# Kernel optimization log

Hardware: AMD Instinct MI355X
Metric: run time of the kernel (lower is better)

Reference implementation:

```python
import jax, jax.numpy as jnp
import numpy as np

HEADS = 16
DIM_HEAD = 64
DIM = 1024
INNER = HEADS * DIM_HEAD  # 1024


def setup_inputs() -> dict:
    key = jax.random.key(0)
    ks = jax.random.split(key, 8)
    B, N, M = 4, 2048, 2048
    x = jax.random.normal(ks[0], (B, N, DIM), dtype=jnp.float32)
    context = jax.random.normal(ks[1], (B, M, DIM), dtype=jnp.float32)
    x_mask = (jax.random.uniform(ks[2], (B, N)) > 0.1).astype(jnp.float32)
    context_mask = (jax.random.uniform(ks[3], (B, M)) > 0.1).astype(jnp.float32)
    s = 0.02
    Wq = jax.random.normal(ks[4], (DIM, INNER), dtype=jnp.float32) * s
    Wkv = jax.random.normal(ks[5], (DIM, 2 * INNER), dtype=jnp.float32) * s
    Wo = jax.random.normal(ks[6], (INNER, DIM), dtype=jnp.float32) * s
    bo = jnp.zeros((DIM,), dtype=jnp.float32)
    return {"x": x, "context": context, "x_mask": x_mask,
            "context_mask": context_mask, "Wq": Wq, "Wkv": Wkv, "Wo": Wo, "bo": bo}


def _split_heads(t):
    b, n, _ = t.shape
    return t.reshape(b, n, HEADS, DIM_HEAD).transpose(0, 2, 1, 3)  # b h n d


def reference(x, context, x_mask, context_mask, Wq, Wkv, Wo, bo):
    scale = DIM_HEAD ** -0.5
    q = _split_heads(x @ Wq)                       # b h n d
    kv = context @ Wkv
    k = _split_heads(kv[..., :INNER])              # b h m d
    v = _split_heads(kv[..., INNER:])              # b h m d
    dots = jnp.einsum('bhnd,bhmd->bhnm', q, k) * scale
    # attn_bias = 1 - x_mask ⊗ context_mask; masked where isclose(attn_bias, 1)
    prod = x_mask[:, None, :, None] * context_mask[:, None, None, :]  # b 1 n m
    masked = jnp.isclose(1.0 - prod, 1.0)          # b 1 n m, broadcast over heads
    dots = jnp.where(masked, -jnp.inf, dots)       # b h n m
    # rows with no valid key: zero the whole row before softmax
    valid = jnp.any(~masked, axis=-1, keepdims=True)  # b 1 n 1
    dots = jnp.where(valid, dots, 0.0)
    attn = jax.nn.softmax(dots, axis=-1)
    attn = jnp.where(valid, attn, 0.0)
    out = jnp.einsum('bhnm,bhmd->bhnd', attn, v)
    b, h, n, d = out.shape
    out = out.transpose(0, 2, 1, 3).reshape(b, n, h * d)
    return out @ Wo + bo
```

## Files before the change

kernel.cpp:

```cpp
#include <hip/hip_runtime.h>

#define DEVI __device__ __forceinline__

typedef __attribute__((ext_vector_type(4))) float f32x4;
typedef __attribute__((ext_vector_type(8))) _Float16 f16x8;
typedef __attribute__((ext_vector_type(2))) _Float16 f16x2;

#if __has_builtin(__builtin_amdgcn_exp2f)
#define EXP2F __builtin_amdgcn_exp2f
#else
#define EXP2F exp2f
#endif

DEVI ushort f2h(float f) {
  _Float16 h = (_Float16)f;
  return __builtin_bit_cast(ushort, h);
}

DEVI unsigned pkrtz(float a, float b) {
  return __builtin_bit_cast(unsigned, __builtin_amdgcn_cvt_pkrtz(a, b));
}

DEVI float dot2acc(unsigned pk, float acc) {
#if __has_builtin(__builtin_amdgcn_fdot2)
  f16x2 one2 = {(_Float16)1.0f, (_Float16)1.0f};
  return __builtin_amdgcn_fdot2(__builtin_bit_cast(f16x2, pk), one2, acc, false);
#else
  f16x2 v = __builtin_bit_cast(f16x2, pk);
  return acc + (float)v[0] + (float)v[1];
#endif
}

DEVI void gload_lds16(const void* g, void* l) {
  typedef const unsigned int GlobU __attribute__((address_space(1)));
  typedef unsigned int LdsU __attribute__((address_space(3)));
  __builtin_amdgcn_global_load_lds((GlobU*)g, (LdsU*)l, 16, 0, 0);
}

__global__ __launch_bounds__(256) void cast_f16_kernel(
    const float4* __restrict__ x, const float4* __restrict__ ctx,
    ushort4* __restrict__ xo, ushort4* __restrict__ co) {
  int i = blockIdx.x * 256 + threadIdx.x;
  const float4* src;
  ushort4* dst;
  int j;
  if (i < 2097152) { src = x; dst = xo; j = i; }
  else             { src = ctx; dst = co; j = i - 2097152; }
  float4 v = src[j];
  ushort4 o;
  o.x = f2h(v.x); o.y = f2h(v.y); o.z = f2h(v.z); o.w = f2h(v.w);
  dst[j] = o;
}

__global__ __launch_bounds__(256) void transpose_cast_kernel(
    const float* __restrict__ Wq, const float* __restrict__ Wkv,
    const float* __restrict__ Wo, ushort* __restrict__ WqT,
    ushort* __restrict__ WkvT, ushort* __restrict__ WoT) {
  __shared__ ushort tile[64][65];
  int bx = blockIdx.x;
  const float* in; ushort* out; int C, cb;
  if (bx < 16)      { in = Wq;  out = WqT;  C = 1024; cb = bx * 64; }
  else if (bx < 48) { in = Wkv; out = WkvT; C = 2048; cb = (bx - 16) * 64; }
  else              { in = Wo;  out = WoT;  C = 1024; cb = (bx - 48) * 64; }
  const int R = 1024;
  int rb = blockIdx.y * 64;
  int t = threadIdx.x;
  int c4 = (t & 15) * 4, r0 = t >> 4;
#pragma unroll
  for (int i = 0; i < 4; i++) {
    int r = r0 + i * 16;
    float4 v = *(const float4*)(in + (size_t)(rb + r) * C + cb + c4);
    tile[r][c4 + 0] = f2h(v.x);
    tile[r][c4 + 1] = f2h(v.y);
    tile[r][c4 + 2] = f2h(v.z);
    tile[r][c4 + 3] = f2h(v.w);
  }
  __syncthreads();
#pragma unroll
  for (int i = 0; i < 4; i++) {
    int rr = r0 + i * 16;
    ushort4 o;
    o.x = tile[c4 + 0][rr]; o.y = tile[c4 + 1][rr];
    o.z = tile[c4 + 2][rr]; o.w = tile[c4 + 3][rr];
    *(ushort4*)(out + (size_t)(cb + rr) * R + rb + c4) = o;
  }
}

DEVI void gemm_stage(const ushort* __restrict__ A, const ushort* __restrict__ Bt,
                     int K, int rowbase, int colbase, int tid, int wave,
                     ushort* AsC, ushort* BsC, int kk) {
#pragma unroll
  for (int i = 0; i < 2; i++) {
    int f = i * 256 + tid;
    int r = f >> 2;
    int c = (f & 3) ^ (r & 3);
    gload_lds16(A + (size_t)(rowbase + r) * K + (kk + c * 8),
                (char*)AsC + (size_t)(i * 256 + wave * 64) * 16);
    gload_lds16(Bt + (size_t)(colbase + r) * K + (kk + c * 8),
                (char*)BsC + (size_t)(i * 256 + wave * 64) * 16);
  }
}

DEVI void gemm_core(const ushort* __restrict__ A, const ushort* __restrict__ Bt,
                    const int K, int rowbase, int colbase, int tid,
                    ushort* As, ushort* Bs, f32x4 acc[4][4]) {
  const int lane = tid & 63, wave = tid >> 6;
  const int quad = lane >> 4, ln = lane & 15;
  const int wrow = (wave >> 1) * 64, wcol = (wave & 1) * 64;

  gemm_stage(A, Bt, K, rowbase, colbase, tid, wave, As, Bs, 0);
  gemm_stage(A, Bt, K, rowbase, colbase, tid, wave, As + 4096, Bs + 4096, 32);

  for (int k0 = 0; k0 < K; k0 += 32) {
    const int cur = (k0 >> 5) & 1;
    ushort* AsC = As + cur * 4096;
    ushort* BsC = Bs + cur * 4096;

    if (k0 + 32 < K) asm volatile("s_waitcnt vmcnt(4)" ::: "memory");
    else             asm volatile("s_waitcnt vmcnt(0)" ::: "memory");
    asm volatile("s_barrier" ::: "memory");

    f16x8 a[4], b[4];
#pragma unroll
    for (int mt = 0; mt < 4; mt++) {
      int r = wrow + mt * 16 + ln;
      a[mt] = *(const f16x8*)(AsC + ((size_t)r * 4 + (quad ^ (r & 3))) * 8);
    }
#pragma unroll
    for (int nt = 0; nt < 4; nt++) {
      int r = wcol + nt * 16 + ln;
      b[nt] = *(const f16x8*)(BsC + ((size_t)r * 4 + (quad ^ (r & 3))) * 8);
    }
#pragma unroll
    for (int mt = 0; mt < 4; mt++)
#pragma unroll
      for (int nt = 0; nt < 4; nt++)
        acc[mt][nt] = __builtin_amdgcn_mfma_f32_16x16x32_f16(a[mt], b[nt], acc[mt][nt], 0, 0, 0);

    asm volatile("s_barrier" ::: "memory");
    if (k0 + 64 < K)
      gemm_stage(A, Bt, K, rowbase, colbase, tid, wave, AsC, BsC, k0 + 64);
  }
}

__global__ __launch_bounds__(256, 3) void qkv_gemm(
    const ushort* __restrict__ xb, const ushort* __restrict__ cb,
    const ushort* __restrict__ WqT, const ushort* __restrict__ WkvT,
    ushort* __restrict__ Qo, ushort* __restrict__ Ko, ushort* __restrict__ Vo) {
  __shared__ ushort As[2 * 128 * 32];
  __shared__ ushort Bs[2 * 128 * 32];
  const int tid = threadIdx.x;
  const int lane = tid & 63, wave = tid >> 6;
  const int quad = lane >> 4, ln = lane & 15;
  const int cy = blockIdx.y;
  const bool isQ = cy < 8;
  const int colbase = (isQ ? cy : cy - 8) * 128;
  const int rowbase = blockIdx.x * 128;
  const int wrow = (wave >> 1) * 64, wcol = (wave & 1) * 64;
  f32x4 acc[4][4] = {};
  gemm_core(isQ ? xb : cb, isQ ? WqT : WkvT, 1024, rowbase, colbase, tid, As, Bs, acc);

  if (isQ) {
    const float qs = 0.18033688011112042f;
#pragma unroll
    for (int nt = 0; nt < 4; nt++) {
      int col = colbase + wcol + nt * 16 + ln;
      int h = col >> 6, d = col & 63;
#pragma unroll
      for (int mt = 0; mt < 4; mt++) {
        int row = rowbase + wrow + mt * 16 + quad * 4;
        int bb = row >> 11, n = row & 2047;
        uint2 pv;
        pv.x = pkrtz(acc[mt][nt][0] * qs, acc[mt][nt][1] * qs);
        pv.y = pkrtz(acc[mt][nt][2] * qs, acc[mt][nt][3] * qs);
        *(uint2*)(Qo + (((size_t)bb * 16 + h) * 64 + d) * 2048 + n) = pv;
      }
    }
  } else {
    bool isK = (colbase < 1024);
#pragma unroll
    for (int nt = 0; nt < 4; nt++) {
      int col = colbase + wcol + nt * 16 + ln;
#pragma unroll
      for (int mt = 0; mt < 4; mt++) {
        int row = rowbase + wrow + mt * 16 + quad * 4;
        int bb = row >> 11, m = row & 2047;
        if (isK) {
          int h = col >> 6, d = col & 63;
#pragma unroll
          for (int r = 0; r < 4; r++)
            Ko[(((size_t)bb * 16 + h) * 2048 + (m + r)) * 64 + d] = f2h(acc[mt][nt][r]);
        } else {
          int c2 = col - 1024;
          int h = c2 >> 6, d = c2 & 63;
          uint2 pv;
          pv.x = pkrtz(acc[mt][nt][0], acc[mt][nt][1]);
          pv.y = pkrtz(acc[mt][nt][2], acc[mt][nt][3]);
          *(uint2*)(Vo + (((size_t)bb * 16 + h) * 64 + d) * 2048 + m) = pv;
        }
      }
    }
  }
}

__global__ __launch_bounds__(256, 3) void out_gemm(
    const ushort* __restrict__ A, const ushort* __restrict__ Bt,
    float* __restrict__ C, const float* __restrict__ bias) {
  __shared__ ushort As[2 * 128 * 32];
  __shared__ ushort Bs[2 * 128 * 32];
  const int tid = threadIdx.x;
  const int lane = tid & 63, wave = tid >> 6;
  const int quad = lane >> 4, ln = lane & 15;
  const int colbase = blockIdx.y * 128, rowbase = blockIdx.x * 128;
  const int wrow = (wave >> 1) * 64, wcol = (wave & 1) * 64;
  f32x4 acc[4][4] = {};
  gemm_core(A, Bt, 1024, rowbase, colbase, tid, As, Bs, acc);
#pragma unroll
  for (int nt = 0; nt < 4; nt++) {
    int col = colbase + wcol + nt * 16 + ln;
    float bv = bias[col];
#pragma unroll
    for (int mt = 0; mt < 4; mt++) {
      int row = rowbase + wrow + mt * 16 + quad * 4;
#pragma unroll
      for (int r = 0; r < 4; r++)
        C[(size_t)(row + r) * 1024 + col] = acc[mt][nt][r] + bv;
    }
  }
}

__global__ __launch_bounds__(512, 4) void attn_kernel(
    const ushort* __restrict__ QT, const ushort* __restrict__ K,
    const ushort* __restrict__ VT, const float* __restrict__ xmask,
    const float* __restrict__ cmask, ushort* __restrict__ O) {
  __shared__ ushort Ks[2][64 * 64];
  __shared__ ushort Vs[2][64 * 64];
  __shared__ ushort Ps[8 * 2048];
  __shared__ float CMB[2048];
  const int tid = threadIdx.x, lane = tid & 63, wave = tid >> 6;
  const int quad = lane >> 4, ln = lane & 15;
  const int bid = blockIdx.x;
  const int qb = bid >> 6, bh6 = bid & 63, h = bh6 & 15, b = bh6 >> 4;
  const size_t bh = (size_t)b * 16 + h;
  const ushort* QTbh = QT + bh * (64 * 2048);
  const ushort* Kbh = K + bh * (2048 * 64);
  const ushort* Vbh = VT + bh * (64 * 2048);
  const int q0 = qb * 256 + wave * 32;

  {
    float4 c0 = *(const float4*)(cmask + b * 2048 + tid * 4);
    float4 b0;
    b0.x = fmaf(c0.x, 3.0e4f, -3.0e4f); b0.y = fmaf(c0.y, 3.0e4f, -3.0e4f);
    b0.z = fmaf(c0.z, 3.0e4f, -3.0e4f); b0.w = fmaf(c0.w, 3.0e4f, -3.0e4f);
    *(float4*)(CMB + tid * 4) = b0;
  }

  f16x8 qf[2][2];
#pragma unroll
  for (int qt = 0; qt < 2; qt++)
#pragma unroll
    for (int kc = 0; kc < 2; kc++) {
      int q = q0 + qt * 16 + ln;
#pragma unroll
      for (int j = 0; j < 8; j++)
        qf[qt][kc][j] = __builtin_bit_cast(_Float16,
            (unsigned short)QTbh[(size_t)(kc * 32 + quad * 8 + j) * 2048 + q]);
    }

  float xm[2];
#pragma unroll
  for (int qt = 0; qt < 2; qt++) xm[qt] = xmask[b * 2048 + q0 + qt * 16 + ln];

  __syncthreads();

  {
    int r = tid >> 3;
    int c = (tid & 7) ^ (r & 7);
#pragma unroll
    for (int t = 0; t < 2; t++) {
      gload_lds16(Kbh + (size_t)(t * 64 + r) * 64 + c * 8, (char*)Ks[t] + (size_t)tid * 16);
      gload_lds16(Vbh + (size_t)r * 2048 + (t * 64 + c * 8), (char*)Vs[t] + (size_t)tid * 16);
    }
  }

  f32x4 o[4][2] = {};
  float lpart[2] = {0.f, 0.f};

  for (int kb = 0; kb < 32; kb++) {
    const int cur = kb & 1;
    const int m0 = kb * 64;
    const ushort* KsC = Ks[cur];
    const ushort* VsC = Vs[cur];

    if (kb < 31) asm volatile("s_waitcnt vmcnt(2)" ::: "memory");
    else         asm volatile("s_waitcnt vmcnt(0)" ::: "memory");
    asm volatile("s_barrier" ::: "memory");

    f32x4 bias4[4];
#pragma unroll
    for (int kt = 0; kt < 4; kt++)
      bias4[kt] = *(const f32x4*)(CMB + m0 + kt * 16 + quad * 4);

    f32x4 s[4][2];
#pragma unroll
    for (int kt = 0; kt < 4; kt++)
#pragma unroll
      for (int qt = 0; qt < 2; qt++) s[kt][qt] = bias4[kt];
#pragma unroll
    for (int kc = 0; kc < 2; kc++) {
#pragma unroll
      for (int kt = 0; kt < 4; kt++) {
        int r = kt * 16 + ln;
        f16x8 ka = *(const f16x8*)(KsC + ((size_t)r * 8 + ((kc * 4 + quad) ^ (r & 7))) * 8);
#pragma unroll
        for (int qt = 0; qt < 2; qt++)
          s[kt][qt] = __builtin_amdgcn_mfma_f32_16x16x32_f16(ka, qf[qt][kc], s[kt][qt], 0, 0, 0);
      }
    }

#pragma unroll
    for (int kc = 0; kc < 2; kc++) {
#pragma unroll
      for (int qt = 0; qt < 2; qt++) {
        ushort* pb = Ps + wave * 2048 + (qt * 2 + kc) * 512;
#pragma unroll
        for (int t = 0; t < 2; t++) {
          int kt = kc * 2 + t;
          float p0 = EXP2F(s[kt][qt][0]);
          float p1 = EXP2F(s[kt][qt][1]);
          float p2 = EXP2F(s[kt][qt][2]);
          float p3 = EXP2F(s[kt][qt][3]);
          uint2 pv;
          pv.x = pkrtz(p0, p1);
          pv.y = pkrtz(p2, p3);
          lpart[qt] = dot2acc(pv.x, lpart[qt]);
          lpart[qt] = dot2acc(pv.y, lpart[qt]);
          *(uint2*)(pb + (t * 2 + (quad >> 1)) * 128 + ln * 8 + (quad & 1) * 4) = pv;
        }
      }
      f16x8 pf[2];
#pragma unroll
      for (int qt = 0; qt < 2; qt++)
        pf[qt] = *(const f16x8*)(Ps + wave * 2048 + (qt * 2 + kc) * 512 + quad * 128 + ln * 8);
#pragma unroll
      for (int dt = 0; dt < 4; dt++) {
        int r = dt * 16 + ln;
        f16x8 va = *(const f16x8*)(VsC + ((size_t)r * 8 + ((kc * 4 + quad) ^ (r & 7))) * 8);
#pragma unroll
        for (int qt = 0; qt < 2; qt++)
          o[dt][qt] = __builtin_amdgcn_mfma_f32_16x16x32_f16(va, pf[qt], o[dt][qt], 0, 0, 0);
      }
    }

    asm volatile("s_barrier" ::: "memory");
    if (kb < 30) {
      const int m2 = m0 + 128;
      int r = tid >> 3;
      int c = (tid & 7) ^ (r & 7);
      gload_lds16(Kbh + (size_t)(m2 + r) * 64 + c * 8, (char*)Ks[cur] + (size_t)tid * 16);
      gload_lds16(Vbh + (size_t)r * 2048 + (m2 + c * 8), (char*)Vs[cur] + (size_t)tid * 16);
    }
  }

#pragma unroll
  for (int qt = 0; qt < 2; qt++) {
    float l = lpart[qt];
    l += __shfl_xor(l, 16, 64);
    l += __shfl_xor(l, 32, 64);
    float inv = (xm[qt] != 0.f && l > 0.f) ? (1.f / l) : 0.f;
    int n = q0 + qt * 16 + ln;
    ushort* ob = O + ((size_t)(b * 2048 + n) * 16 + h) * 64;
#pragma unroll
    for (int dt = 0; dt < 4; dt++) {
      uint2 pv;
      pv.x = pkrtz(o[dt][qt][0] * inv, o[dt][qt][1] * inv);
      pv.y = pkrtz(o[dt][qt][2] * inv, o[dt][qt][3] * inv);
      *(uint2*)(ob + dt * 16 + quad * 4) = pv;
    }
  }
}

extern "C" void kernel_launch(void* const* d_in, const int* in_sizes, int n_in,
                              void* d_out, int out_size, void* d_ws, size_t ws_size,
                              hipStream_t stream) {
  const float* x   = (const float*)d_in[0];
  const float* ctx = (const float*)d_in[1];
  const float* xm  = (const float*)d_in[2];
  const float* cm  = (const float*)d_in[3];
  const float* Wq  = (const float*)d_in[4];
  const float* Wkv = (const float*)d_in[5];
  const float* Wo  = (const float*)d_in[6];
  const float* bo  = (const float*)d_in[7];

  char* ws = (char*)d_ws;
  const size_t MB = 1024 * 1024;
  ushort* xb   = (ushort*)(ws + 0);
  ushort* cb   = (ushort*)(ws + 16 * MB);
  ushort* WqT  = (ushort*)(ws + 32 * MB);
  ushort* WkvT = (ushort*)(ws + 34 * MB);
  ushort* WoT  = (ushort*)(ws + 38 * MB);
  ushort* QTb  = (ushort*)(ws + 40 * MB);
  ushort* Kb   = (ushort*)(ws + 56 * MB);
  ushort* VTb  = (ushort*)(ws + 72 * MB);
  ushort* Ob   = xb;

  cast_f16_kernel<<<16384, 256, 0, stream>>>((const float4*)x, (const float4*)ctx,
                                             (ushort4*)xb, (ushort4*)cb);
  transpose_cast_kernel<<<dim3(64, 16), 256, 0, stream>>>(Wq, Wkv, Wo, WqT, WkvT, WoT);
  qkv_gemm<<<dim3(64, 24), 256, 0, stream>>>(xb, cb, WqT, WkvT, QTb, Kb, VTb);
  attn_kernel<<<512, 512, 0, stream>>>(QTb, Kb, VTb, xm, cm, Ob);
  out_gemm<<<dim3(64, 8), 256, 0, stream>>>(Ob, WoT, (float*)d_out, bo);
}
```

Baseline: 312.2 us.

## Permute K row order so softmax probabilities stay in registers for PV MFMA

Loads K tiles into LDS with a permuted row order, and adjusts the column-mask bias indexing to match, so the S=K·Q MFMA output layout lines up with the B-operand layout the P·V MFMA expects. This removes the per-wave LDS round trip for the probability tile (the Ps buffer, its stores and reloads) and frees 32 KB of shared memory. The cost is extra index arithmetic for the permuted rows, and correctness depends on the permutation exactly matching the MFMA fragment layout.

```diff
diff --git a/kernel.cpp b/kernel.cpp
--- a/kernel.cpp
+++ b/kernel.cpp
@@ -5,6 +5,7 @@
 typedef __attribute__((ext_vector_type(4))) float f32x4;
 typedef __attribute__((ext_vector_type(8))) _Float16 f16x8;
 typedef __attribute__((ext_vector_type(2))) _Float16 f16x2;
+typedef __attribute__((ext_vector_type(4))) unsigned u32x4;
 
 #if __has_builtin(__builtin_amdgcn_exp2f)
 #define EXP2F __builtin_amdgcn_exp2f
@@ -235,7 +236,6 @@
     const float* __restrict__ cmask, ushort* __restrict__ O) {
   __shared__ ushort Ks[2][64 * 64];
   __shared__ ushort Vs[2][64 * 64];
-  __shared__ ushort Ps[8 * 2048];
   __shared__ float CMB[2048];
   const int tid = threadIdx.x, lane = tid & 63, wave = tid >> 6;
   const int quad = lane >> 4, ln = lane & 15;
@@ -273,14 +273,14 @@
 
   __syncthreads();
 
-  {
-    int r = tid >> 3;
-    int c = (tid & 7) ^ (r & 7);
-#pragma unroll
-    for (int t = 0; t < 2; t++) {
-      gload_lds16(Kbh + (size_t)(t * 64 + r) * 64 + c * 8, (char*)Ks[t] + (size_t)tid * 16);
-      gload_lds16(Vbh + (size_t)r * 2048 + (t * 64 + c * 8), (char*)Vs[t] + (size_t)tid * 16);
-    }
+  const int sr = tid >> 3;
+  const int sc = (tid & 7) ^ (sr & 7);
+  const int srp = (sr & 32) | ((sr & 12) << 1) | ((sr & 16) >> 2) | (sr & 3);
+
+#pragma unroll
+  for (int t = 0; t < 2; t++) {
+    gload_lds16(Kbh + (size_t)(t * 64 + srp) * 64 + sc * 8, (char*)Ks[t] + (size_t)tid * 16);
+    gload_lds16(Vbh + (size_t)sr * 2048 + (t * 64 + sc * 8), (char*)Vs[t] + (size_t)tid * 16);
   }
 
   f32x4 o[4][2] = {};
@@ -299,7 +299,7 @@
     f32x4 bias4[4];
 #pragma unroll
     for (int kt = 0; kt < 4; kt++)
-      bias4[kt] = *(const f32x4*)(CMB + m0 + kt * 16 + quad * 4);
+      bias4[kt] = *(const f32x4*)(CMB + m0 + (kt >> 1) * 32 + quad * 8 + (kt & 1) * 4);
 
     f32x4 s[4][2];
 #pragma unroll
@@ -320,28 +320,22 @@
 
 #pragma unroll
     for (int kc = 0; kc < 2; kc++) {
+      f16x8 pf[2];
 #pragma unroll
       for (int qt = 0; qt < 2; qt++) {
-        ushort* pb = Ps + wave * 2048 + (qt * 2 + kc) * 512;
-#pragma unroll
-        for (int t = 0; t < 2; t++) {
-          int kt = kc * 2 + t;
-          float p0 = EXP2F(s[kt][qt][0]);
-          float p1 = EXP2F(s[kt][qt][1]);
-          float p2 = EXP2F(s[kt][qt][2]);
-          float p3 = EXP2F(s[kt][qt][3]);
-          uint2 pv;
-          pv.x = pkrtz(p0, p1);
-          pv.y = pkrtz(p2, p3);
-          lpart[qt] = dot2acc(pv.x, lpart[qt]);
-          lpart[qt] = dot2acc(pv.y, lpart[qt]);
-          *(uint2*)(pb + (t * 2 + (quad >> 1)) * 128 + ln * 8 + (quad & 1) * 4) = pv;
-        }
+        f32x4 sA = s[kc * 2 + 0][qt];
+        f32x4 sB = s[kc * 2 + 1][qt];
+        u32x4 u;
+        u[0] = pkrtz(EXP2F(sA[0]), EXP2F(sA[1]));
+        u[1] = pkrtz(EXP2F(sA[2]), EXP2F(sA[3]));
+        u[2] = pkrtz(EXP2F(sB[0]), EXP2F(sB[1]));
+        u[3] = pkrtz(EXP2F(sB[2]), EXP2F(sB[3]));
+        lpart[qt] = dot2acc(u[0], lpart[qt]);
+        lpart[qt] = dot2acc(u[1], lpart[qt]);
+        lpart[qt] = dot2acc(u[2], lpart[qt]);
+        lpart[qt] = dot2acc(u[3], lpart[qt]);
+        pf[qt] = __builtin_bit_cast(f16x8, u);
       }
-      f16x8 pf[2];
-#pragma unroll
-      for (int qt = 0; qt < 2; qt++)
-        pf[qt] = *(const f16x8*)(Ps + wave * 2048 + (qt * 2 + kc) * 512 + quad * 128 + ln * 8);
 #pragma unroll
       for (int dt = 0; dt < 4; dt++) {
         int r = dt * 16 + ln;
@@ -355,10 +349,8 @@
     asm volatile("s_barrier" ::: "memory");
     if (kb < 30) {
       const int m2 = m0 + 128;
-      int r = tid >> 3;
-      int c = (tid & 7) ^ (r & 7);
-      gload_lds16(Kbh + (size_t)(m2 + r) * 64 + c * 8, (char*)Ks[cur] + (size_t)tid * 16);
-      gload_lds16(Vbh + (size_t)r * 2048 + (m2 + c * 8), (char*)Vs[cur] + (size_t)tid * 16);
+      gload_lds16(Kbh + (size_t)(m2 + srp) * 64 + sc * 8, (char*)Ks[cur] + (size_t)tid * 16);
+      gload_lds16(Vbh + (size_t)sr * 2048 + (m2 + sc * 8), (char*)Vs[cur] + (size_t)tid * 16);
     }
   }
 
```

Result: no change. 306.6 us (-1.8%).
